# Kernel tuning notes

Measured on AMD Instinct MI355X. Metric: run time of the kernel, lower is better.

The kernel has to match this reference:

```python
import jax, jax.numpy as jnp
import numpy as np

B, N, TD, SD, BD, K, M, TOPK, H = 8, 1024, 5120, 2048, 1024, 16, 4, 2, 8
HD = SD // H  # 256


def _ln(x, g, b, eps=1e-5):
    m = jnp.mean(x, -1, keepdims=True)
    v = jnp.mean((x - m) ** 2, -1, keepdims=True)
    return (x - m) * jax.lax.rsqrt(v + eps) * g + b


def _adapter(h, dw, db, uw, ub, lg, lb, q, wq, bq, wk, bk, wv, bv, ow, ob, pg, pb):
    # bottleneck trunk: down -> GELU -> up -> LN (dropout = identity in eval)
    x = jax.nn.gelu(h @ dw + db, approximate=False)          # [B,N,BD]
    x = _ln(x @ uw + ub, lg, lb)                             # [B,N,SD]
    Bb = x.shape[0]
    # cross-attention: learnable queries [K,SD] attend over x
    qp = (q @ wq + bq).reshape(K, H, HD).transpose(1, 0, 2)                      # [H,K,HD]
    kp = (x @ wk + bk).reshape(Bb, -1, H, HD).transpose(0, 2, 1, 3)              # [B,H,N,HD]
    vp = (x @ wv + bv).reshape(Bb, -1, H, HD).transpose(0, 2, 1, 3)              # [B,H,N,HD]
    att = jax.nn.softmax(jnp.einsum('hkd,bhnd->bhkn', qp, kp) * (1.0 / np.sqrt(HD)), axis=-1)
    ctx = jnp.einsum('bhkn,bhnd->bhkd', att, vp).transpose(0, 2, 1, 3).reshape(Bb, K, SD)
    ctx = ctx @ ow + ob
    return _ln(ctx + q[None], pg, pb)                        # residual with queries


def setup_inputs():
    key = jax.random.key(0)
    it = iter(jax.random.split(key, 40))
    def nrm(shape, s=0.02):
        return jax.random.normal(next(it), shape, jnp.float32) * s
    inp = {'h_teacher': jax.random.normal(next(it), (B, N, TD), jnp.float32)}
    for pre, lead in (('g_', ()), ('s_', (M,))):
        inp[pre + 'dw'] = nrm(lead + (TD, BD)); inp[pre + 'db'] = jnp.zeros(lead + (BD,), jnp.float32)
        inp[pre + 'uw'] = nrm(lead + (BD, SD)); inp[pre + 'ub'] = jnp.zeros(lead + (SD,), jnp.float32)
        inp[pre + 'lg'] = jnp.ones(lead + (SD,), jnp.float32); inp[pre + 'lb'] = jnp.zeros(lead + (SD,), jnp.float32)
        inp[pre + 'q'] = nrm(lead + (K, SD))
        for nm in ('wq', 'wk', 'wv', 'ow'):
            inp[pre + nm] = nrm(lead + (SD, SD))
        for nm in ('bq', 'bk', 'bv', 'ob'):
            inp[pre + nm] = jnp.zeros(lead + (SD,), jnp.float32)
        inp[pre + 'pg'] = jnp.ones(lead + (SD,), jnp.float32); inp[pre + 'pb'] = jnp.zeros(lead + (SD,), jnp.float32)
    inp['r_w1'] = nrm((TD, 512)); inp['r_b1'] = jnp.zeros((512,), jnp.float32)
    inp['r_w2'] = nrm((512, M)); inp['r_b2'] = jnp.zeros((M,), jnp.float32)
    return inp


def reference(h_teacher, g_dw, g_db, g_uw, g_ub, g_lg, g_lb, g_q, g_wq, g_bq, g_wk, g_bk, g_wv, g_bv, g_ow, g_ob, g_pg, g_pb, s_dw, s_db, s_uw, s_ub, s_lg, s_lb, s_q, s_wq, s_bq, s_wk, s_bk, s_wv, s_bv, s_ow, s_ob, s_pg, s_pb, r_w1, r_b1, r_w2, r_b2):
    # generalized adapter (always on)
    c_g = _adapter(h_teacher, g_dw, g_db, g_uw, g_ub, g_lg, g_lb, g_q, g_wq, g_bq, g_wk, g_bk, g_wv, g_bv, g_ow, g_ob, g_pg, g_pb)
    # all specialized experts computed densely (as the torch module does), then gathered
    c_spec = jax.vmap(lambda dw, db, uw, ub, lg, lb, q, wq, bq, wk, bk, wv, bv, ow, ob, pg, pb:
                      _adapter(h_teacher, dw, db, uw, ub, lg, lb, q, wq, bq, wk, bk, wv, bv, ow, ob, pg, pb))(
        s_dw, s_db, s_uw, s_ub, s_lg, s_lb, s_q, s_wq, s_bq, s_wk, s_bk, s_wv, s_bv, s_ow, s_ob, s_pg, s_pb)  # [M,B,K,SD]
    cs = jnp.transpose(c_spec, (1, 0, 2, 3))                 # [B,M,K,SD]
    # router on mean-pooled teacher summary (eval: no noise)
    pooled = jnp.mean(h_teacher, axis=1)                     # [B,TD]
    logits = jax.nn.gelu(pooled @ r_w1 + r_b1, approximate=False) @ r_w2 + r_b2
    probs = jax.nn.softmax(logits, axis=-1)                  # [B,M]
    w, idx = jax.lax.top_k(probs, TOPK)                      # [B,TOPK]
    w = w / (jnp.sum(w, -1, keepdims=True) + 1e-8)
    sel = cs[jnp.arange(cs.shape[0])[:, None], idx]          # [B,TOPK,K,SD]
    c_s = jnp.sum(sel * w[:, :, None, None], axis=1)         # [B,K,SD]
    c_agg = jnp.concatenate([c_g, c_s], axis=1)              # [B,2K,SD]
    return c_agg, probs
```

## Files before the change

### kernel.cpp

```cpp
#include <hip/hip_runtime.h>
#include <hip/hip_bf16.h>

#define B_   8
#define N_   1024
#define TD_  5120
#define SD_  2048
#define BD_  1024
#define K_   16
#define H_   8

typedef unsigned short u16;
typedef __attribute__((ext_vector_type(8))) short bf16x8;
typedef __attribute__((ext_vector_type(4))) float f32x4;
typedef __attribute__((ext_vector_type(8))) u16 u16x8;

__device__ __forceinline__ float bf2f(u16 u) {
    union { unsigned int i; float f; } x; x.i = ((unsigned)u) << 16; return x.f;
}
__device__ __forceinline__ u16 f2bf(float f) {
    union { float f; unsigned int i; } x; x.f = f;
    unsigned int i = x.i;
    return (u16)((i + 0x7fffu + ((i >> 16) & 1u)) >> 16);
}
__device__ __forceinline__ float gelu_exact(float v) {
    return 0.5f * v * (1.0f + erff(v * 0.70710678118654752f));
}
__device__ __forceinline__ void gload_lds16(const void* g, void* l) {
    __builtin_amdgcn_global_load_lds(
        (const __attribute__((address_space(1))) unsigned int*)g,
        (__attribute__((address_space(3))) unsigned int*)l, 16, 0, 0);
}

struct Ptr5 { const float* p[5]; };
struct Ptr40 { const float* p[8][5]; };

template<int EPI, int AMODE>
__global__ __launch_bounds__(512, 2)
void gemm256(const u16* __restrict__ Abase,
             const u16* __restrict__ Bbase, long bStride,
             const float* __restrict__ biasBase, int biasStride,
             u16* __restrict__ Cbase, int ldc, long cStride, int Kd,
             const int* __restrict__ units_a, const int* __restrict__ units_b)
{
    __shared__ char lds[131072];
    const int u = blockIdx.z;
    const int ua = units_a[u];
    const int ub = (AMODE == 0) ? units_b[u] : u;
    const u16* A  = Abase + (size_t)ub * 1024 * Kd;
    const u16* Bt = Bbase + (size_t)ua * bStride;
    const float* bias = biasBase + (size_t)ua * biasStride;
    u16* C = Cbase + (size_t)u * cStride;

    const int tid  = threadIdx.x;
    const int wave = tid >> 6, lane = tid & 63;
    const int wm = wave >> 2, wn = wave & 3;
    const int row0 = blockIdx.x * 256, col0 = blockIdx.y * 256;

    const int srow = tid >> 3;
    const int scol = ((tid & 7) ^ ((tid >> 3) & 7)) << 3;
    const char* aSrc = (const char*)(A  + (size_t)(row0 + srow) * Kd + scol);
    const char* bSrc = (const char*)(Bt + (size_t)(col0 + srow) * Kd + scol);
    const int ldsW = wave * 1024;

    const int fr = lane & 15, fq = lane >> 4;
    const int kl  = fq << 4;
    const int swz = (fr & 7) << 4;

    f32x4 acc[8][4] = {};
    bf16x8 aF[8], bF[4];

#define STAGE_A(bufv, hh, kt) do { \
    const char* s_ = aSrc + ((size_t)((hh)*128) * Kd + (size_t)(kt) * 64) * 2; \
    char* d_ = lds + (bufv)*65536 + (hh)*16384 + ldsW; \
    gload_lds16(s_, d_); \
    gload_lds16(s_ + (size_t)64 * Kd * 2, d_ + 8192); } while(0)
#define STAGE_B(bufv, hh, kt) do { \
    const char* s_ = bSrc + ((size_t)((hh)*128) * Kd + (size_t)(kt) * 64) * 2; \
    char* d_ = lds + (bufv)*65536 + 32768 + (hh)*16384 + ldsW; \
    gload_lds16(s_, d_); \
    gload_lds16(s_ + (size_t)64 * Kd * 2, d_ + 8192); } while(0)

#define LDA_(bufv, mf, kk) (*(const bf16x8*)(lds + (bufv)*65536 + \
    ((mf)*32 + wm*16 + fr)*128 + ((((kk)*64) + kl) ^ swz)))
#define LDB_(bufv, nf, kk) (*(const bf16x8*)(lds + (bufv)*65536 + 32768 + \
    (wn*64 + (nf)*16 + fr)*128 + ((((kk)*64) + kl) ^ swz)))

#define FENCE_ asm volatile("" ::: "memory")
#define BAR_   __builtin_amdgcn_s_barrier()
#define WAITL_ asm volatile("s_waitcnt lgkmcnt(0)" ::: "memory")
#define VM_(n) asm volatile("s_waitcnt vmcnt(" #n ")" ::: "memory")

#define READ_B(bufv, kk) { _Pragma("unroll") \
    for (int n_ = 0; n_ < 4; ++n_) bF[n_] = LDB_(bufv, n_, kk); }
#define READ_A8(bufv, kk) { _Pragma("unroll") \
    for (int i_ = 0; i_ < 8; ++i_) aF[i_] = LDA_(bufv, i_, kk); }
#define MFMA32_ { __builtin_amdgcn_s_setprio(1); \
    _Pragma("unroll") for (int i_ = 0; i_ < 8; ++i_) { \
      _Pragma("unroll") for (int n_ = 0; n_ < 4; ++n_) \
        acc[i_][n_] = __builtin_amdgcn_mfma_f32_16x16x32_bf16( \
            aF[i_], bF[n_], acc[i_][n_], 0, 0, 0); } \
    __builtin_amdgcn_s_setprio(0); }

    STAGE_A(0, 0, 0); STAGE_A(0, 1, 0);
    STAGE_B(0, 0, 0); STAGE_B(0, 1, 0);

    const int nt = Kd >> 6;
    for (int T = 0; T < nt - 1; ++T) {
        const int bufv = T & 1, nb = bufv ^ 1;
        STAGE_A(nb, 0, T + 1); STAGE_A(nb, 1, T + 1);
        VM_(4); BAR_; FENCE_;
        READ_B(bufv, 0); READ_A8(bufv, 0);
        STAGE_B(nb, 0, T + 1); STAGE_B(nb, 1, T + 1);
        WAITL_; MFMA32_;
        READ_B(bufv, 1); READ_A8(bufv, 1);
        WAITL_; MFMA32_;
        BAR_;
    }
    {
        const int bufv = (nt - 1) & 1;
        VM_(0); BAR_; FENCE_;
        READ_B(bufv, 0); READ_A8(bufv, 0);
        WAITL_; MFMA32_;
        READ_B(bufv, 1); READ_A8(bufv, 1);
        WAITL_; MFMA32_;
    }

#undef STAGE_A
#undef STAGE_B
#undef LDA_
#undef LDB_
#undef FENCE_
#undef BAR_
#undef WAITL_
#undef VM_
#undef READ_B
#undef READ_A8
#undef MFMA32_

#pragma unroll
    for (int mf = 0; mf < 8; ++mf)
#pragma unroll
        for (int nf = 0; nf < 4; ++nf) {
            const int col = col0 + wn*64 + nf*16 + fr;
            const float bv = bias[col];
#pragma unroll
            for (int j = 0; j < 4; ++j) {
                const int row = row0 + mf*32 + wm*16 + fq*4 + j;
                float v = acc[mf][nf][j] + bv;
                if (EPI == 1) v = gelu_exact(v);
                C[(size_t)row*ldc + col] = f2bf(v);
            }
        }
}

__global__ void cvt_bf16_flat(const float* __restrict__ in, u16* __restrict__ out, long n8) {
    long i = (long)blockIdx.x * blockDim.x + threadIdx.x;
    const long stride = (long)gridDim.x * blockDim.x;
    for (; i < n8; i += stride) {
        const f32x4* p = (const f32x4*)in + i*2;
        f32x4 a = p[0], b = p[1];
        u16x8 o;
        o[0]=f2bf(a[0]); o[1]=f2bf(a[1]); o[2]=f2bf(a[2]); o[3]=f2bf(a[3]);
        o[4]=f2bf(b[0]); o[5]=f2bf(b[1]); o[6]=f2bf(b[2]); o[7]=f2bf(b[3]);
        ((u16x8*)out)[i] = o;
    }
}

__global__ __launch_bounds__(256)
void cvt_transpose(const float* __restrict__ W, u16* __restrict__ Wt, int Kd, int Nd) {
    __shared__ float t[64][65];
    const int k0 = blockIdx.x * 64, n0 = blockIdx.y * 64;
    const int tid = threadIdx.x;
#pragma unroll
    for (int i = 0; i < 4; ++i) {
        int ch = tid + i*256;
        int r = ch >> 4, c4 = (ch & 15) << 2;
        f32x4 v = *(const f32x4*)(W + (size_t)(k0 + r)*Nd + n0 + c4);
        t[r][c4] = v[0]; t[r][c4+1] = v[1]; t[r][c4+2] = v[2]; t[r][c4+3] = v[3];
    }
    __syncthreads();
#pragma unroll
    for (int i = 0; i < 2; ++i) {
        int ch = tid + i*256;
        int nr = ch >> 3, c8 = (ch & 7) << 3;
        u16x8 o;
#pragma unroll
        for (int j = 0; j < 8; ++j) o[j] = f2bf(t[c8 + j][nr]);
        *(u16x8*)(Wt + (size_t)(n0 + nr)*Kd + k0 + c8) = o;
    }
}

__global__ __launch_bounds__(256)
void ln_rows_u(u16* __restrict__ X, const float* __restrict__ gslab,
               const float* __restrict__ bslab, const int* __restrict__ units_a) {
    const int row = blockIdx.x, tid = threadIdx.x;
    const int ua = units_a[row >> 10];
    const float* g  = gslab + (size_t)ua*SD_;
    const float* bt = bslab + (size_t)ua*SD_;
    u16* rp = X + (size_t)row*SD_;
    const u16x8 v = ((const u16x8*)rp)[tid];
    float f[8]; float s = 0.f, s2 = 0.f;
#pragma unroll
    for (int j = 0; j < 8; ++j) { f[j] = bf2f(v[j]); s += f[j]; s2 += f[j]*f[j]; }
    __shared__ float sa[4], sb[4];
#pragma unroll
    for (int o = 32; o > 0; o >>= 1) { s += __shfl_down(s, o); s2 += __shfl_down(s2, o); }
    if ((tid & 63) == 0) { sa[tid >> 6] = s; sb[tid >> 6] = s2; }
    __syncthreads();
    s = sa[0]+sa[1]+sa[2]+sa[3]; s2 = sb[0]+sb[1]+sb[2]+sb[3];
    const float mean = s * (1.0f/SD_);
    const float inv  = rsqrtf(s2 * (1.0f/SD_) - mean*mean + 1e-5f);
    const int c0 = tid*8;
    u16x8 o;
#pragma unroll
    for (int j = 0; j < 8; ++j) o[j] = f2bf((f[j]-mean)*inv*g[c0+j] + bt[c0+j]);
    ((u16x8*)rp)[tid] = o;
}

__global__ __launch_bounds__(256)
void qp_part(Ptr5 q, Ptr5 wq, float* __restrict__ Sp) {
    __shared__ float qL[16][256];
    const int a = blockIdx.y, ks = blockIdx.z;
    const int c = blockIdx.x*256 + threadIdx.x;
    const int t = threadIdx.x;
    const float* Q = q.p[a];
    for (int i = t; i < 16*256; i += 256)
        qL[i >> 8][i & 255] = Q[(size_t)(i >> 8)*SD_ + ks*256 + (i & 255)];
    __syncthreads();
    const float* W = wq.p[a] + (size_t)(ks*256)*SD_ + c;
    float acc[16] = {};
    for (int i = 0; i < 256; i += 4) {
        const float w0 = W[(size_t)i*SD_];
        const float w1 = W[(size_t)(i+1)*SD_];
        const float w2 = W[(size_t)(i+2)*SD_];
        const float w3 = W[(size_t)(i+3)*SD_];
#pragma unroll
        for (int k = 0; k < 16; ++k) {
            f32x4 q4 = *(const f32x4*)&qL[k][i];
            acc[k] += q4[0]*w0 + q4[1]*w1 + q4[2]*w2 + q4[3]*w3;
        }
    }
#pragma unroll
    for (int k = 0; k < 16; ++k)
        Sp[((size_t)(a*8 + ks)*16 + k)*SD_ + c] = acc[k];
}

__global__ void qp_reduce(const float* __restrict__ Sp, Ptr5 bq, float* __restrict__ qp) {
    const int idx = blockIdx.x*256 + threadIdx.x;
    const int a = idx >> 15, k = (idx >> 11) & 15, c = idx & 2047;
    float s = bq.p[a][c];
#pragma unroll
    for (int ks = 0; ks < 8; ++ks)
        s += Sp[((size_t)(a*8 + ks)*16 + k)*SD_ + c];
    qp[idx] = s;
}

__global__ __launch_bounds__(256)
void scores_sm(const u16* __restrict__ Kb, const float* __restrict__ qp,
               const int* __restrict__ units_a, float* __restrict__ P)
{
    __shared__ float sL[16][1024];
    __shared__ float qL[16][256];
    __shared__ float red[8];
    const int u = blockIdx.x >> 3, hh = blockIdx.x & 7;
    const int ua = units_a[u];
    const int t = threadIdx.x;
    for (int i = t; i < 16*256; i += 256)
        qL[i >> 8][i & 255] = qp[(size_t)(ua*16 + (i >> 8))*SD_ + hh*256 + (i & 255)];
    __syncthreads();
    const u16* Ku = Kb + (size_t)u*1024*SD_ + hh*256;
#pragma unroll
    for (int j = 0; j < 4; ++j) {
        const int n = t + j*256;
        const u16* kr = Ku + (size_t)n*SD_;
        float acc[16] = {};
        for (int d0 = 0; d0 < 256; d0 += 8) {
            u16x8 kv8 = *(const u16x8*)(kr + d0);
            float kf[8];
#pragma unroll
            for (int e = 0; e < 8; ++e) kf[e] = bf2f(kv8[e]);
#pragma unroll
            for (int k = 0; k < 16; ++k) {
                f32x4 q0 = *(const f32x4*)&qL[k][d0];
                f32x4 q1 = *(const f32x4*)&qL[k][d0+4];
                acc[k] += q0[0]*kf[0] + q0[1]*kf[1] + q0[2]*kf[2] + q0[3]*kf[3]
                        + q1[0]*kf[4] + q1[1]*kf[5] + q1[2]*kf[6] + q1[7==7?7:7]*kf[7];
            }
        }
#pragma unroll
        for (int k = 0; k < 16; ++k) sL[k][n] = acc[k] * 0.0625f;
    }
    __syncthreads();
    const int lane = t & 63, wv = t >> 6;
    for (int k = 0; k < 16; ++k) {
        float v0 = sL[k][t], v1 = sL[k][t+256], v2 = sL[k][t+512], v3 = sL[k][t+768];
        float mx = fmaxf(fmaxf(v0,v1), fmaxf(v2,v3));
#pragma unroll
        for (int o = 1; o < 64; o <<= 1) mx = fmaxf(mx, __shfl_xor(mx, o));
        if (lane == 0) red[wv] = mx;
        __syncthreads();
        mx = fmaxf(fmaxf(red[0],red[1]), fmaxf(red[2],red[3]));
        float e0 = expf(v0-mx), e1 = expf(v1-mx), e2 = expf(v2-mx), e3 = expf(v3-mx);
        float s = e0+e1+e2+e3;
#pragma unroll
        for (int o = 1; o < 64; o <<= 1) s += __shfl_xor(s, o);
        if (lane == 0) red[4+wv] = s;
        __syncthreads();
        s = red[4]+red[5]+red[6]+red[7];
        const float inv = 1.0f/s;
        float* Pr = P + ((size_t)(u*8+hh)*16 + k)*1024;
        Pr[t]=e0*inv; Pr[t+256]=e1*inv; Pr[t+512]=e2*inv; Pr[t+768]=e3*inv;
        __syncthreads();
    }
}

__global__ __launch_bounds__(256)
void ctx_u(const u16* __restrict__ Vb, const float* __restrict__ P,
           u16* __restrict__ ctxb)
{
    __shared__ float pL[16][1024];
    const int u = blockIdx.x >> 3, hh = blockIdx.x & 7;
    const int t = threadIdx.x;
    const float* Pu = P + (size_t)(u*8+hh)*16*1024;
    for (int i = t; i < 16*1024/4; i += 256)
        ((f32x4*)&pL[0][0])[i] = ((const f32x4*)Pu)[i];
    __syncthreads();
    const u16* Vu = Vb + (size_t)u*1024*SD_ + hh*256 + t;
    float acc[16] = {};
    for (int n = 0; n < 1024; n += 4) {
        float vv0 = bf2f(Vu[(size_t)n*SD_]);
        float vv1 = bf2f(Vu[(size_t)(n+1)*SD_]);
        float vv2 = bf2f(Vu[(size_t)(n+2)*SD_]);
        float vv3 = bf2f(Vu[(size_t)(n+3)*SD_]);
#pragma unroll
        for (int k = 0; k < 16; ++k) {
            f32x4 p4 = *(const f32x4*)&pL[k][n];
            acc[k] += p4[0]*vv0 + p4[1]*vv1 + p4[2]*vv2 + p4[3]*vv3;
        }
    }
#pragma unroll
    for (int k = 0; k < 16; ++k)
        ctxb[(size_t)u*16*SD_ + k*SD_ + hh*256 + t] = f2bf(acc[k]);
}

__global__ __launch_bounds__(256)
void gemm_ow(const u16* __restrict__ ctxb, const u16* __restrict__ Bslab,
             const float* __restrict__ biasSlab, const int* __restrict__ units_a,
             float* __restrict__ ctx2)
{
    const int u = blockIdx.y, ua = units_a[u];
    const int wave = threadIdx.x >> 6, lane = threadIdx.x & 63;
    const int col0 = blockIdx.x*256 + wave*64;
    const u16* A  = ctxb + (size_t)u*16*SD_;
    const u16* Bt = Bslab + (size_t)ua*SD_*SD_;
    const int fr = lane & 15, fk8 = (lane >> 4) << 3;
    f32x4 acc[4] = {};
    for (int k0 = 0; k0 < SD_; k0 += 32) {
        bf16x8 af = *(const bf16x8*)(A + (size_t)fr*SD_ + k0 + fk8);
#pragma unroll
        for (int n = 0; n < 4; ++n) {
            bf16x8 bf8 = *(const bf16x8*)(Bt + (size_t)(col0 + n*16 + fr)*SD_ + k0 + fk8);
            acc[n] = __builtin_amdgcn_mfma_f32_16x16x32_bf16(af, bf8, acc[n], 0, 0, 0);
        }
    }
    const int fq = lane >> 4;
#pragma unroll
    for (int n = 0; n < 4; ++n)
#pragma unroll
        for (int j = 0; j < 4; ++j) {
            const int row = fq*4 + j, col = col0 + n*16 + fr;
            ctx2[(size_t)u*16*SD_ + (size_t)row*SD_ + col] = acc[n][j] + biasSlab[ua*SD_ + col];
        }
}

__global__ __launch_bounds__(256)
void ln_post_u(const float* __restrict__ ctx2, const float* __restrict__ qslab,
               const float* __restrict__ pgs, const float* __restrict__ pbs,
               const int* __restrict__ units_a, const int* __restrict__ units_b,
               float* __restrict__ out, float* __restrict__ cspec)
{
    const int k = blockIdx.x, u = blockIdx.y, tid = threadIdx.x;
    const int ua = units_a[u];
    const float* ip = ctx2 + ((size_t)u*16 + k)*SD_;
    const float* qr = qslab + ((size_t)ua*16 + k)*SD_;
    const float* g  = pgs + (size_t)ua*SD_;
    const float* bt = pbs + (size_t)ua*SD_;
    float f[8]; float s = 0.f, s2 = 0.f;
#pragma unroll
    for (int j = 0; j < 8; ++j) {
        const int c = tid + j*256;
        f[j] = ip[c] + qr[c];
        s += f[j]; s2 += f[j]*f[j];
    }
    __shared__ float sa[4], sb[4];
#pragma unroll
    for (int o = 32; o > 0; o >>= 1) { s += __shfl_down(s, o); s2 += __shfl_down(s2, o); }
    if ((tid & 63) == 0) { sa[tid >> 6] = s; sb[tid >> 6] = s2; }
    __syncthreads();
    s = sa[0]+sa[1]+sa[2]+sa[3]; s2 = sb[0]+sb[1]+sb[2]+sb[3];
    const float mean = s * (1.0f/SD_);
    const float inv  = rsqrtf(s2 * (1.0f/SD_) - mean*mean + 1e-5f);
    float* op = (u < 8) ? out + ((size_t)units_b[u]*32 + k)*SD_
                        : cspec + ((size_t)(u-8)*16 + k)*SD_;
#pragma unroll
    for (int j = 0; j < 8; ++j) { const int c = tid + j*256; op[c] = (f[j]-mean)*inv*g[c] + bt[c]; }
}

__global__ __launch_bounds__(256)
void pool_part(const float* __restrict__ h, float* __restrict__ pp) {
    const int c = blockIdx.x*256 + threadIdx.x;
    const int b = blockIdx.y, ns = blockIdx.z;
    const float* p = h + ((size_t)b*N_ + ns*256)*TD_ + c;
    float s = 0.f;
    for (int n = 0; n < 256; ++n) s += p[(size_t)n*TD_];
    pp[(size_t)ns*8*TD_ + (size_t)b*TD_ + c] = s;
}
__global__ void pool_reduce(const float* __restrict__ pp, float* __restrict__ pooled) {
    const int idx = blockIdx.x*256 + threadIdx.x;
    const float s = pp[idx] + pp[idx + 8*TD_] + pp[idx + 16*TD_] + pp[idx + 24*TD_];
    pooled[idx] = s * (1.0f/N_);
}

__global__ __launch_bounds__(256)
void rmlp_part(const float* __restrict__ pooled, const float* __restrict__ w1,
               float* __restrict__ rp) {
    const int c = blockIdx.x*256 + threadIdx.x;
    const int b = blockIdx.y, is = blockIdx.z;
    const float* pr = pooled + b*TD_ + is*512;
    const float* W = w1 + (size_t)(is*512)*512 + c;
    float s = 0.f;
    for (int i = 0; i < 512; ++i) s += pr[i] * W[(size_t)i*512];
    rp[(b*10 + is)*512 + c] = s;
}
__global__ void rmlp_reduce(const float* __restrict__ rp, const float* __restrict__ b1,
                            float* __restrict__ hid) {
    const int idx = blockIdx.x*256 + threadIdx.x;
    const int b = idx >> 9, c = idx & 511;
    float s = b1[c];
#pragma unroll
    for (int is = 0; is < 10; ++is) s += rp[(b*10 + is)*512 + c];
    hid[idx] = gelu_exact(s);
}

__global__ void router_final(const float* __restrict__ hid, const float* __restrict__ w2,
                             const float* __restrict__ b2, float* __restrict__ probs,
                             int* __restrict__ widx, float* __restrict__ wval,
                             int* __restrict__ units_a, int* __restrict__ units_b) {
    __shared__ float lg[8][4];
    __shared__ int sw[16];
    const int tid = threadIdx.x;
    if (tid < 32) {
        const int b = tid >> 2, m = tid & 3;
        float s = b2[m];
        const float* hr = hid + b*512;
        for (int i = 0; i < 512; ++i) s += hr[i]*w2[i*4 + m];
        lg[b][m] = s;
    }
    __syncthreads();
    if (tid < 8) {
        const int b = tid;
        const float l0=lg[b][0], l1=lg[b][1], l2=lg[b][2], l3=lg[b][3];
        const float mx = fmaxf(fmaxf(l0,l1),fmaxf(l2,l3));
        const float e0=expf(l0-mx), e1=expf(l1-mx), e2=expf(l2-mx), e3=expf(l3-mx);
        const float s = e0+e1+e2+e3;
        float p[4] = {e0/s, e1/s, e2/s, e3/s};
        probs[b*4+0]=p[0]; probs[b*4+1]=p[1]; probs[b*4+2]=p[2]; probs[b*4+3]=p[3];
        int i0 = 0;
        for (int m = 1; m < 4; ++m) if (p[m] > p[i0]) i0 = m;
        int i1 = -1;
        for (int m = 0; m < 4; ++m) if (m != i0 && (i1 < 0 || p[m] > p[i1])) i1 = m;
        const float w0 = p[i0], w1 = p[i1], ws = w0 + w1 + 1e-8f;
        widx[b*2]=i0; widx[b*2+1]=i1;
        wval[b*2]=w0/ws; wval[b*2+1]=w1/ws;
        sw[b*2]=i0; sw[b*2+1]=i1;
    }
    __syncthreads();
    if (tid < 24) {
        units_a[tid] = (tid < 8) ? 0 : sw[tid-8] + 1;
        units_b[tid] = (tid < 8) ? tid : ((tid-8) >> 1);
    }
}

__global__ void combine_k(const float* __restrict__ cspec, const int* __restrict__ widx,
                          const float* __restrict__ wval, float* __restrict__ out) {
    const int i = blockIdx.x*256 + threadIdx.x;
    const int c4 = i & 511;
    const int k  = (i >> 9) & 15;
    const int b  = i >> 13;
    const float w0 = wval[b*2], w1 = wval[b*2+1];
    const f32x4 v0 = ((const f32x4*)cspec)[(size_t)((2*b)  *16 + k)*512 + c4];
    const f32x4 v1 = ((const f32x4*)cspec)[(size_t)((2*b+1)*16 + k)*512 + c4];
    ((f32x4*)out)[(size_t)(b*32 + 16 + k)*512 + c4] = v0*w0 + v1*w1;
}

__global__ void pack5(Ptr5 src, float* __restrict__ dst, int len) {
    int i = blockIdx.x*256 + threadIdx.x;
    if (i < 5*len) dst[i] = src.p[i/len][i%len];
}
__global__ void pack_slab8(Ptr40 s, float* __restrict__ dst) {
    int i = blockIdx.x*256 + threadIdx.x;
    int slab = i / 10240, rem = i % 10240;
    dst[i] = s.p[slab][rem / 2048][rem % 2048];
}

extern "C" void kernel_launch(void* const* d_in, const int* in_sizes, int n_in,
                              void* d_out, int out_size, void* d_ws, size_t ws_size,
                              hipStream_t stream) {
    if (ws_size < 300300000ULL) return;

    const float* h = (const float*)d_in[0];
    const float* G[17]; const float* Sx[17];
    for (int i = 0; i < 17; ++i) { G[i] = (const float*)d_in[1+i]; Sx[i] = (const float*)d_in[18+i]; }
    const float* r_w1 = (const float*)d_in[35];
    const float* r_b1 = (const float*)d_in[36];
    const float* r_w2 = (const float*)d_in[37];
    const float* r_b2 = (const float*)d_in[38];

    static const size_t str[17] = {
        (size_t)TD_*BD_, BD_, (size_t)BD_*SD_, SD_, SD_, SD_, (size_t)K_*SD_,
        (size_t)SD_*SD_, (size_t)SD_*SD_, (size_t)SD_*SD_, (size_t)SD_*SD_,
        SD_, SD_, SD_, SD_, SD_, SD_ };
    auto P = [&](int pi, int a) -> const float* {
        return (a == 0) ? G[pi] : Sx[pi] + (size_t)(a-1)*str[pi];
    };

    char* w = (char*)d_ws;
    const size_t R0 = 0, R1 = 100663296, R2 = 201326592, R3 = 251658240, TAIL = 293601280;
    u16*   h_bf  = (u16*)(w + R0);
    u16*   X     = (u16*)(w + R0);
    u16*   wt_dw = (u16*)(w + R1);
    u16*   Kbuf  = (u16*)(w + R1);
    u16*   X1    = (u16*)(w + R2);
    u16*   wt_v  = (u16*)(w + R2);
    u16*   wt_ow = (u16*)(w + R2);
    u16*   wt_uw = (u16*)(w + R3);
    u16*   wt_k  = (u16*)(w + R3);
    u16*   ctxb  = (u16*)(w + R3);
    float* ctx2  = (float*)(w + R3 + 1572864);
    float* cspec = (float*)(w + R3 + 4718592);
    float* Pbuf  = (float*)(w + R3 + 6815744);
    float* qpp   = (float*)(w + R2);
    float* poolp = (float*)(w + R2 + 12582912);
    float* routp = (float*)(w + R2 + 14680064);
    float* qp_all  = (float*)(w + TAIL);
    float* qslab   = (float*)(w + TAIL + 655360);
    float* bias_dw = (float*)(w + TAIL + 1310720);
    float* slab8   = (float*)(w + TAIL + 1331200);
    float* pooled  = (float*)(w + TAIL + 1658880);
    float* hid     = (float*)(w + TAIL + 1822720);
    int*   widx    = (int*)  (w + TAIL + 1839104);
    float* wval    = (float*)(w + TAIL + 1839168);
    int*   units_a = (int*)  (w + TAIL + 1839232);
    int*   units_b = (int*)  (w + TAIL + 1839328);

    float* bias_uw = slab8;
    float* bias_k  = slab8 + 1*5*SD_;
    float* bias_v  = slab8 + 2*5*SD_;
    float* bias_ow = slab8 + 3*5*SD_;
    float* lng     = slab8 + 4*5*SD_;
    float* lnb     = slab8 + 5*5*SD_;
    float* pgs     = slab8 + 6*5*SD_;
    float* pbs     = slab8 + 7*5*SD_;

    float* out = (float*)d_out;

    cvt_bf16_flat<<<2048, 256, 0, stream>>>(h, h_bf, (long)((size_t)B_*N_*TD_/8));
    pool_part<<<dim3(20, 8, 4), 256, 0, stream>>>(h, poolp);
    pool_reduce<<<160, 256, 0, stream>>>(poolp, pooled);
    rmlp_part<<<dim3(2, 8, 10), 256, 0, stream>>>(pooled, r_w1, routp);
    rmlp_reduce<<<16, 256, 0, stream>>>(routp, r_b1, hid);
    router_final<<<1, 64, 0, stream>>>(hid, r_w2, r_b2, out + 524288, widx, wval, units_a, units_b);

    Ptr5 q5, wq5, bq5, db5;
    for (int a = 0; a < 5; ++a) { q5.p[a]=P(6,a); wq5.p[a]=P(7,a); bq5.p[a]=P(11,a); db5.p[a]=P(1,a); }
    qp_part<<<dim3(8, 5, 8), 256, 0, stream>>>(q5, wq5, qpp);
    qp_reduce<<<640, 256, 0, stream>>>(qpp, bq5, qp_all);
    pack5<<<20, 256, 0, stream>>>(db5, bias_dw, BD_);
    pack5<<<640, 256, 0, stream>>>(q5, qslab, 16*SD_);
    Ptr40 s8;
    static const int slab_pi[8] = {3, 12, 13, 14, 4, 5, 15, 16};
    for (int si = 0; si < 8; ++si)
        for (int a = 0; a < 5; ++a) s8.p[si][a] = P(slab_pi[si], a);
    pack_slab8<<<320, 256, 0, stream>>>(s8, slab8);

    for (int a = 0; a < 5; ++a) {
        cvt_transpose<<<dim3(TD_/64, BD_/64), 256, 0, stream>>>(P(0,a), wt_dw + (size_t)a*BD_*TD_, TD_, BD_);
        cvt_transpose<<<dim3(BD_/64, SD_/64), 256, 0, stream>>>(P(2,a), wt_uw + (size_t)a*SD_*BD_, BD_, SD_);
    }

    gemm256<1, 0><<<dim3(4, 4, 24), 512, 0, stream>>>(
        h_bf, wt_dw, (long)BD_*TD_, bias_dw, BD_, X1, BD_, (long)1024*BD_, TD_, units_a, units_b);

    gemm256<0, 1><<<dim3(4, 8, 24), 512, 0, stream>>>(
        X1, wt_uw, (long)SD_*BD_, bias_uw, SD_, X, SD_, (long)1024*SD_, BD_, units_a, units_b);

    ln_rows_u<<<24*1024, 256, 0, stream>>>(X, lng, lnb, units_a);

    for (int a = 0; a < 5; ++a) {
        cvt_transpose<<<dim3(SD_/64, SD_/64), 256, 0, stream>>>(P(8,a), wt_k + (size_t)a*SD_*SD_, SD_, SD_);
        cvt_transpose<<<dim3(SD_/64, SD_/64), 256, 0, stream>>>(P(9,a), wt_v + (size_t)a*SD_*SD_, SD_, SD_);
    }

    gemm256<0, 1><<<dim3(4, 8, 24), 512, 0, stream>>>(
        X, wt_k, (long)SD_*SD_, bias_k, SD_, Kbuf, SD_, (long)1024*SD_, SD_, units_a, units_b);

    scores_sm<<<24*8, 256, 0, stream>>>(Kbuf, qp_all, units_a, Pbuf);

    gemm256<0, 1><<<dim3(4, 8, 24), 512, 0, stream>>>(
        X, wt_v, (long)SD_*SD_, bias_v, SD_, Kbuf, SD_, (long)1024*SD_, SD_, units_a, units_b);

    for (int a = 0; a < 5; ++a)
        cvt_transpose<<<dim3(SD_/64, SD_/64), 256, 0, stream>>>(P(10,a), wt_ow + (size_t)a*SD_*SD_, SD_, SD_);

    ctx_u<<<24*8, 256, 0, stream>>>(Kbuf, Pbuf, ctxb);

    gemm_ow<<<dim3(8, 24), 256, 0, stream>>>(ctxb, wt_ow, bias_ow, units_a, ctx2);

    ln_post_u<<<dim3(16, 24), 256, 0, stream>>>(ctx2, qslab, pgs, pbs, units_a, units_b, out, cspec);
    combine_k<<<256, 256, 0, stream>>>(cspec, widx, wval, out);
}
```

Measured before the change: 1.361 ms.

## Add 128-tile GEMM for down-proj, fuse bf16 cast with pooling, reorder grid

Adds a new 128x128-tile, 256-thread GEMM kernel with a simple single-buffered LDS loop and uses it for the large down-projection (K=5120), aiming for more blocks in flight and higher occupancy than the 256-tile kernel. The bf16 conversion of the teacher activations is fused with the mean-pool partial sums, so the large input is read once instead of twice. The grid of the remaining 256-tile GEMMs is reordered so the unit index is the fastest-varying block dimension, which changes L2 reuse of weights and activations. The new GEMM has no double buffering, so load latency is exposed on each K step, and the pool reduction now sums 128 partials per column.

```diff
diff --git a/kernel.cpp b/kernel.cpp
--- a/kernel.cpp
+++ b/kernel.cpp
@@ -13,6 +13,7 @@
 typedef __attribute__((ext_vector_type(8))) short bf16x8;
 typedef __attribute__((ext_vector_type(4))) float f32x4;
 typedef __attribute__((ext_vector_type(8))) u16 u16x8;
+typedef __attribute__((ext_vector_type(4))) u16 u16x4;
 
 __device__ __forceinline__ float bf2f(u16 u) {
     union { unsigned int i; float f; } x; x.i = ((unsigned)u) << 16; return x.f;
@@ -33,6 +34,92 @@
 
 struct Ptr5 { const float* p[5]; };
 struct Ptr40 { const float* p[8][5]; };
+
+template<int EPI, int AMODE>
+__global__ __launch_bounds__(256, 4)
+void gemm128(const u16* __restrict__ Abase,
+             const u16* __restrict__ Bbase, long bStride,
+             const float* __restrict__ biasBase, int biasStride,
+             u16* __restrict__ Cbase, int ldc, long cStride, int Kd,
+             const int* __restrict__ units_a, const int* __restrict__ units_b)
+{
+    __shared__ char lds[32768];
+    const int u = blockIdx.x;
+    const int ua = units_a[u];
+    const int ub = (AMODE == 0) ? units_b[u] : u;
+    const u16* A  = Abase + (size_t)ub * 1024 * Kd;
+    const u16* Bt = Bbase + (size_t)ua * bStride;
+    const float* bias = biasBase + (size_t)ua * biasStride;
+    u16* C = Cbase + (size_t)u * cStride;
+
+    const int tid  = threadIdx.x;
+    const int wave = tid >> 6, lane = tid & 63;
+    const int wm = wave >> 1, wn = wave & 1;
+    const int row0 = blockIdx.z * 128, col0 = blockIdx.y * 128;
+
+    const int srow = tid >> 3;
+    const int scol = ((tid & 7) ^ (srow & 7)) << 3;
+    const char* aSrc = (const char*)(A  + (size_t)(row0 + srow) * Kd + scol);
+    const char* bSrc = (const char*)(Bt + (size_t)(col0 + srow) * Kd + scol);
+    const int ldsW = wave * 1024;
+
+    const int fr = lane & 15, fq = lane >> 4;
+    const int kl  = fq << 4;
+    const int swz = (fr & 7) << 4;
+
+    f32x4 acc[4][4] = {};
+
+#define LDA_(mf, kk) (*(const bf16x8*)(lds + \
+    (wm*64 + (mf)*16 + fr)*128 + ((((kk)*64) + kl) ^ swz)))
+#define LDB_(nf, kk) (*(const bf16x8*)(lds + 16384 + \
+    (wn*64 + (nf)*16 + fr)*128 + ((((kk)*64) + kl) ^ swz)))
+
+    const int nt = Kd >> 6;
+    for (int T = 0; T < nt; ++T) {
+        const size_t kb = (size_t)T << 7;
+#pragma unroll
+        for (int l = 0; l < 4; ++l)
+            gload_lds16(aSrc + (size_t)(l*32)*Kd*2 + kb, lds + l*4096 + ldsW);
+#pragma unroll
+        for (int l = 0; l < 4; ++l)
+            gload_lds16(bSrc + (size_t)(l*32)*Kd*2 + kb, lds + 16384 + l*4096 + ldsW);
+        asm volatile("s_waitcnt vmcnt(0)" ::: "memory");
+        __syncthreads();
+#pragma unroll
+        for (int kk = 0; kk < 2; ++kk) {
+            bf16x8 aF[4], bF[4];
+#pragma unroll
+            for (int i = 0; i < 4; ++i) aF[i] = LDA_(i, kk);
+#pragma unroll
+            for (int n = 0; n < 4; ++n) bF[n] = LDB_(n, kk);
+#pragma unroll
+            for (int i = 0; i < 4; ++i)
+#pragma unroll
+                for (int n = 0; n < 4; ++n)
+                    acc[i][n] = __builtin_amdgcn_mfma_f32_16x16x32_bf16(
+                        aF[i], bF[n], acc[i][n], 0, 0, 0);
+        }
+        __syncthreads();
+    }
+
+#undef LDA_
+#undef LDB_
+
+#pragma unroll
+    for (int mf = 0; mf < 4; ++mf)
+#pragma unroll
+        for (int nf = 0; nf < 4; ++nf) {
+            const int col = col0 + wn*64 + nf*16 + fr;
+            const float bv = bias[col];
+#pragma unroll
+            for (int j = 0; j < 4; ++j) {
+                const int row = row0 + wm*64 + mf*16 + fq*4 + j;
+                float v = acc[mf][nf][j] + bv;
+                if (EPI == 1) v = gelu_exact(v);
+                C[(size_t)row*ldc + col] = f2bf(v);
+            }
+        }
+}
 
 template<int EPI, int AMODE>
 __global__ __launch_bounds__(512, 2)
@@ -43,7 +130,7 @@
              const int* __restrict__ units_a, const int* __restrict__ units_b)
 {
     __shared__ char lds[131072];
-    const int u = blockIdx.z;
+    const int u = blockIdx.x;
     const int ua = units_a[u];
     const int ub = (AMODE == 0) ? units_b[u] : u;
     const u16* A  = Abase + (size_t)ub * 1024 * Kd;
@@ -54,7 +141,7 @@
     const int tid  = threadIdx.x;
     const int wave = tid >> 6, lane = tid & 63;
     const int wm = wave >> 2, wn = wave & 3;
-    const int row0 = blockIdx.x * 256, col0 = blockIdx.y * 256;
+    const int row0 = blockIdx.z * 256, col0 = blockIdx.y * 256;
 
     const int srow = tid >> 3;
     const int scol = ((tid & 7) ^ ((tid >> 3) & 7)) << 3;
@@ -153,17 +240,38 @@
         }
 }
 
-__global__ void cvt_bf16_flat(const float* __restrict__ in, u16* __restrict__ out, long n8) {
-    long i = (long)blockIdx.x * blockDim.x + threadIdx.x;
-    const long stride = (long)gridDim.x * blockDim.x;
-    for (; i < n8; i += stride) {
-        const f32x4* p = (const f32x4*)in + i*2;
-        f32x4 a = p[0], b = p[1];
-        u16x8 o;
-        o[0]=f2bf(a[0]); o[1]=f2bf(a[1]); o[2]=f2bf(a[2]); o[3]=f2bf(a[3]);
-        o[4]=f2bf(b[0]); o[5]=f2bf(b[1]); o[6]=f2bf(b[2]); o[7]=f2bf(b[3]);
-        ((u16x8*)out)[i] = o;
-    }
+__global__ __launch_bounds__(256)
+void cvt_pool(const float* __restrict__ h, u16* __restrict__ hb,
+              float* __restrict__ pp) {
+    const int b = blockIdx.x, nc = blockIdx.y, t = threadIdx.x;
+    const float* hp = h + ((size_t)b*N_ + (size_t)nc*8)*TD_;
+    u16* op = hb + ((size_t)b*N_ + (size_t)nc*8)*TD_;
+    f32x4 sum[5] = {};
+    for (int r = 0; r < 8; ++r) {
+        const float* rp = hp + (size_t)r*TD_;
+        u16* orow = op + (size_t)r*TD_;
+#pragma unroll
+        for (int j = 0; j < 5; ++j) {
+            const int c = (t + 256*j) << 2;
+            f32x4 v = *(const f32x4*)(rp + c);
+            sum[j] += v;
+            u16x4 o = { f2bf(v[0]), f2bf(v[1]), f2bf(v[2]), f2bf(v[3]) };
+            *(u16x4*)(orow + c) = o;
+        }
+    }
+#pragma unroll
+    for (int j = 0; j < 5; ++j) {
+        const int c = (t + 256*j) << 2;
+        *(f32x4*)(pp + ((size_t)b*128 + nc)*TD_ + c) = sum[j];
+    }
+}
+
+__global__ void pool_reduce(const float* __restrict__ pp, float* __restrict__ pooled) {
+    const int idx = blockIdx.x*256 + threadIdx.x;
+    const int b = idx / TD_, c = idx % TD_;
+    float s = 0.f;
+    for (int nc = 0; nc < 128; ++nc) s += pp[((size_t)b*128 + nc)*TD_ + c];
+    pooled[idx] = s * (1.0f/N_);
 }
 
 __global__ __launch_bounds__(256)
@@ -284,7 +392,7 @@
                 f32x4 q0 = *(const f32x4*)&qL[k][d0];
                 f32x4 q1 = *(const f32x4*)&qL[k][d0+4];
                 acc[k] += q0[0]*kf[0] + q0[1]*kf[1] + q0[2]*kf[2] + q0[3]*kf[3]
-                        + q1[0]*kf[4] + q1[1]*kf[5] + q1[2]*kf[6] + q1[7==7?7:7]*kf[7];
+                        + q1[0]*kf[4] + q1[1]*kf[5] + q1[2]*kf[6] + q1[3]*kf[7];
             }
         }
 #pragma unroll
@@ -404,21 +512,6 @@
                         : cspec + ((size_t)(u-8)*16 + k)*SD_;
 #pragma unroll
     for (int j = 0; j < 8; ++j) { const int c = tid + j*256; op[c] = (f[j]-mean)*inv*g[c] + bt[c]; }
-}
-
-__global__ __launch_bounds__(256)
-void pool_part(const float* __restrict__ h, float* __restrict__ pp) {
-    const int c = blockIdx.x*256 + threadIdx.x;
-    const int b = blockIdx.y, ns = blockIdx.z;
-    const float* p = h + ((size_t)b*N_ + ns*256)*TD_ + c;
-    float s = 0.f;
-    for (int n = 0; n < 256; ++n) s += p[(size_t)n*TD_];
-    pp[(size_t)ns*8*TD_ + (size_t)b*TD_ + c] = s;
-}
-__global__ void pool_reduce(const float* __restrict__ pp, float* __restrict__ pooled) {
-    const int idx = blockIdx.x*256 + threadIdx.x;
-    const float s = pp[idx] + pp[idx + 8*TD_] + pp[idx + 16*TD_] + pp[idx + 24*TD_];
-    pooled[idx] = s * (1.0f/N_);
 }
 
 __global__ __launch_bounds__(256)
@@ -541,7 +634,7 @@
     float* Pbuf  = (float*)(w + R3 + 6815744);
     float* qpp   = (float*)(w + R2);
     float* poolp = (float*)(w + R2 + 12582912);
-    float* routp = (float*)(w + R2 + 14680064);
+    float* routp = (float*)(w + R2 + 33554432);
     float* qp_all  = (float*)(w + TAIL);
     float* qslab   = (float*)(w + TAIL + 655360);
     float* bias_dw = (float*)(w + TAIL + 1310720);
@@ -564,8 +657,7 @@
 
     float* out = (float*)d_out;
 
-    cvt_bf16_flat<<<2048, 256, 0, stream>>>(h, h_bf, (long)((size_t)B_*N_*TD_/8));
-    pool_part<<<dim3(20, 8, 4), 256, 0, stream>>>(h, poolp);
+    cvt_pool<<<dim3(8, 128), 256, 0, stream>>>(h, h_bf, poolp);
     pool_reduce<<<160, 256, 0, stream>>>(poolp, pooled);
     rmlp_part<<<dim3(2, 8, 10), 256, 0, stream>>>(pooled, r_w1, routp);
     rmlp_reduce<<<16, 256, 0, stream>>>(routp, r_b1, hid);
@@ -588,10 +680,10 @@
         cvt_transpose<<<dim3(BD_/64, SD_/64), 256, 0, stream>>>(P(2,a), wt_uw + (size_t)a*SD_*BD_, BD_, SD_);
     }
 
-    gemm256<1, 0><<<dim3(4, 4, 24), 512, 0, stream>>>(
+    gemm128<1, 0><<<dim3(24, 8, 8), 256, 0, stream>>>(
         h_bf, wt_dw, (long)BD_*TD_, bias_dw, BD_, X1, BD_, (long)1024*BD_, TD_, units_a, units_b);
 
-    gemm256<0, 1><<<dim3(4, 8, 24), 512, 0, stream>>>(
+    gemm256<0, 1><<<dim3(24, 8, 4), 512, 0, stream>>>(
         X1, wt_uw, (long)SD_*BD_, bias_uw, SD_, X, SD_, (long)1024*SD_, BD_, units_a, units_b);
 
     ln_rows_u<<<24*1024, 256, 0, stream>>>(X, lng, lnb, units_a);
@@ -601,12 +693,12 @@
         cvt_transpose<<<dim3(SD_/64, SD_/64), 256, 0, stream>>>(P(9,a), wt_v + (size_t)a*SD_*SD_, SD_, SD_);
     }
 
-    gemm256<0, 1><<<dim3(4, 8, 24), 512, 0, stream>>>(
+    gemm256<0, 1><<<dim3(24, 8, 4), 512, 0, stream>>>(
         X, wt_k, (long)SD_*SD_, bias_k, SD_, Kbuf, SD_, (long)1024*SD_, SD_, units_a, units_b);
 
     scores_sm<<<24*8, 256, 0, stream>>>(Kbuf, qp_all, units_a, Pbuf);
 
-    gemm256<0, 1><<<dim3(4, 8, 24), 512, 0, stream>>>(
+    gemm256<0, 1><<<dim3(24, 8, 4), 512, 0, stream>>>(
         X, wt_v, (long)SD_*SD_, bias_v, SD_, Kbuf, SD_, (long)1024*SD_, SD_, units_a, units_b);
 
     for (int a = 0; a < 5; ++a)
```

After: 1.375 ms. No clear change (+1.1%).
